# Kernel optimization log

Measured on AMD Instinct MI355X. Metric: run time of the kernel, lower is better.

## Reference

```python
import jax, jax.numpy as jnp
import numpy as np

N = 100000   # nodes
E = 3200000  # edges
F = 128      # num_features
H = 32       # hidden
G = 512      # graphs in batch


def setup_inputs() -> dict:
    key = jax.random.key(0)
    ks = jax.random.split(key, 6)
    x = jax.random.normal(ks[0], (N, F), dtype=jnp.float32)
    edge_index = jax.random.randint(ks[1], (2, E), 0, N, dtype=jnp.int32)
    batch = jnp.sort(jax.random.randint(ks[2], (N,), 0, G, dtype=jnp.int32))
    W1 = jax.random.normal(ks[3], (F, H), dtype=jnp.float32) * 0.05
    b1 = jnp.zeros((H,), dtype=jnp.float32)
    Wg = jax.random.normal(ks[4], (3 * H, 1), dtype=jnp.float32) * 0.05
    bg = jnp.zeros((1,), dtype=jnp.float32)
    return {"x": x, "edge_index": edge_index, "batch": batch,
            "W1": W1, "b1": b1, "Wg": Wg, "bg": bg}


def gcn_conv(x, W, b, edge_index, n):
    # PyG GCNConv: linear transform, add self-loops, symmetric normalization, scatter-add, bias
    h = x @ W  # [N, H]
    loop = jnp.arange(n, dtype=edge_index.dtype)
    src = jnp.concatenate([edge_index[0], loop])
    dst = jnp.concatenate([edge_index[1], loop])
    deg = jax.ops.segment_sum(jnp.ones_like(dst, dtype=h.dtype), dst, num_segments=n)
    dinv = jnp.where(deg > 0, jax.lax.rsqrt(deg), 0.0)
    norm = dinv[src] * dinv[dst]  # [E+N]
    msg = h[src] * norm[:, None]  # gather + scale
    out = jax.ops.segment_sum(msg, dst, num_segments=n)  # scatter-add
    return out + b


def reference(x, edge_index, batch, W1, b1, Wg, bg):
    h = gcn_conv(x, W1, b1, edge_index, N)  # [N, 32]
    h = jax.nn.relu(h)
    s = jax.ops.segment_sum(h, batch, num_segments=G)          # global_add_pool
    cnt = jax.ops.segment_sum(jnp.ones((N, 1), h.dtype), batch, num_segments=G)
    m = s / jnp.maximum(cnt, 1.0)                              # global_mean_pool
    mx = jax.ops.segment_max(h, batch, num_segments=G)         # global_max_pool
    mx = jnp.where(cnt > 0, mx, 0.0)
    g = jnp.concatenate([s, m, mx], axis=1)  # [G, 96]
    return g @ Wg + bg  # [G, 1]
```

## Files before the change

### kernel.cpp

```cpp
#include <hip/hip_runtime.h>
#include <hip/hip_fp16.h>

#define NN 100000
#define NE 3200000
#define NF 128
#define NH 32
#define NG 512
#define NR 196
#define RSZ 512
#define CAP 17408
#define EPB 8192
#define NBE 391
#define PNB 782
#define PRSZ 128

typedef int   v4i __attribute__((ext_vector_type(4)));
typedef float v4f __attribute__((ext_vector_type(4)));

__device__ __forceinline__ __half2 shfl_xor_h2(__half2 v, int m) {
    int iv = *(int*)&v;
    int r = __shfl_xor(iv, m);
    return *(__half2*)&r;
}

__global__ __launch_bounds__(256) void k_cscatter(const int* __restrict__ src,
                                                  const int* __restrict__ dst,
                                                  int* __restrict__ ccur,
                                                  unsigned int* __restrict__ cbucket) {
    __shared__ int h[NR];
    __shared__ int basev[NR];
    for (int i = threadIdx.x; i < NR; i += 256) h[i] = 0;
    __syncthreads();
    int base = blockIdx.x * EPB;
    int lim = NE - base;
    int4 dv[8], sv[8];
    int valid[8];
#pragma unroll
    for (int k = 0; k < 8; ++k) {
        int idx = threadIdx.x + k * 256;
        valid[k] = (idx * 4 < lim);
        if (valid[k]) {
            dv[k] = ((const int4*)(dst + base))[idx];
            sv[k] = ((const int4*)(src + base))[idx];
            atomicAdd(&h[dv[k].x >> 9], 1);
            atomicAdd(&h[dv[k].y >> 9], 1);
            atomicAdd(&h[dv[k].z >> 9], 1);
            atomicAdd(&h[dv[k].w >> 9], 1);
        }
    }
    __syncthreads();
    for (int i = threadIdx.x; i < NR; i += 256) {
        int c = h[i];
        basev[i] = c ? (i * CAP + atomicAdd(&ccur[i], c)) : 0;
    }
    __syncthreads();
    for (int i = threadIdx.x; i < NR; i += 256) h[i] = 0;
    __syncthreads();
#pragma unroll
    for (int k = 0; k < 8; ++k) {
        if (valid[k]) {
            int d, s, r, p;
#define EMIT(DD, SS) d = (DD); s = (SS); r = d >> 9; \
            p = basev[r] + atomicAdd(&h[r], 1); \
            cbucket[p] = (unsigned int)(((d & 511) << 17) | s);
            EMIT(dv[k].x, sv[k].x)
            EMIT(dv[k].y, sv[k].y)
            EMIT(dv[k].z, sv[k].z)
            EMIT(dv[k].w, sv[k].w)
#undef EMIT
        }
    }
}

__global__ __launch_bounds__(256) void k_cscan(const int* __restrict__ ccur,
                                               int* __restrict__ cptr) {
    int t = threadIdx.x;
    int own = (t < NR) ? ccur[t] : 0;
    __shared__ int part[256];
    part[t] = own;
    __syncthreads();
    for (int off = 1; off < 256; off <<= 1) {
        int v = (t >= off) ? part[t - off] : 0;
        __syncthreads();
        part[t] += v;
        __syncthreads();
    }
    if (t < NR) cptr[t] = part[t] - own;
    if (t == 0) cptr[NR] = NE;
}

__global__ __launch_bounds__(512) void k_rangesort(const int* __restrict__ cptr,
                                                   const unsigned int* __restrict__ cbucket,
                                                   int* __restrict__ row_ptr,
                                                   int* __restrict__ bucket,
                                                   float* __restrict__ dinv) {
    __shared__ int h[RSZ];
    __shared__ int lptr[RSZ];
    int r = blockIdx.x;
    int obeg = cptr[r];
    int cnt = cptr[r + 1] - obeg;
    int ibeg = r * CAP;
    int t = threadIdx.x;
    h[t] = 0;
    __syncthreads();
    for (int i = t; i < cnt; i += RSZ)
        atomicAdd(&h[cbucket[ibeg + i] >> 17], 1);
    __syncthreads();
    lptr[t] = h[t];
    __syncthreads();
    for (int off = 1; off < RSZ; off <<= 1) {
        int v = (t >= off) ? lptr[t - off] : 0;
        __syncthreads();
        lptr[t] += v;
        __syncthreads();
    }
    int node0 = r * RSZ;
    int v = node0 + t;
    if (v < NN) {
        int ex = lptr[t] - h[t];
        row_ptr[v] = obeg + ex;
        dinv[v] = rsqrtf((float)(h[t] + 1));
    }
    __syncthreads();
    h[t] = lptr[t] - h[t];
    __syncthreads();
    for (int i = t; i < cnt; i += RSZ) {
        unsigned int w = cbucket[ibeg + i];
        int off_ = atomicAdd(&h[w >> 17], 1);
        bucket[obeg + off_] = (int)(w & 0x1FFFF);
    }
    if (r == 0 && t == 0) row_ptr[NN] = NE;
}

__global__ __launch_bounds__(256) void k_gemm(const float* __restrict__ x,
                                              const float* __restrict__ W1,
                                              const float* __restrict__ dinv,
                                              __half* __restrict__ hs) {
    __shared__ float sW[NF][NH];
    __shared__ float sX[32][NF + 4];
    int t = threadIdx.x;
    const float4* W4 = (const float4*)W1;
    float4* sW4 = (float4*)&sW[0][0];
#pragma unroll
    for (int i = 0; i < 4; ++i) sW4[t + 256 * i] = W4[t + 256 * i];

    long row0 = (long)blockIdx.x * 32;
    const float* xb = x + row0 * NF;
#pragma unroll
    for (int i = 0; i < 4; ++i) {
        int idx4 = t + 256 * i;
        int r = idx4 >> 5;
        int c = (idx4 & 31) * 4;
        v4f v = __builtin_nontemporal_load((const v4f*)(xb + idx4 * 4));
        sX[r][c] = v.x; sX[r][c + 1] = v.y; sX[r][c + 2] = v.z; sX[r][c + 3] = v.w;
    }
    __syncthreads();

    int r = t >> 3;
    int c = (t & 7) * 4;
    float4 acc = {0.f, 0.f, 0.f, 0.f};
#pragma unroll 8
    for (int k = 0; k < NF; ++k) {
        float xv = sX[r][k];
        float4 w = *(const float4*)&sW[k][c];
        acc.x += xv * w.x; acc.y += xv * w.y;
        acc.z += xv * w.z; acc.w += xv * w.w;
    }
    float dv = dinv[row0 + r];
    __half2 h01 = __floats2half2_rn(acc.x * dv, acc.y * dv);
    __half2 h23 = __floats2half2_rn(acc.z * dv, acc.w * dv);
    uint2 packed = { *(unsigned int*)&h01, *(unsigned int*)&h23 };
    *(uint2*)&hs[(row0 + r) * NH + c] = packed;
}

__global__ __launch_bounds__(256) void k_gath(
    const int* __restrict__ row_ptr, const int* __restrict__ bucket,
    const __half* __restrict__ hs, const float* __restrict__ dinv,
    const float* __restrict__ b1, __half* __restrict__ nodeout) {
    int wave = threadIdx.x >> 6;
    int lane = threadIdx.x & 63;
    int fq = lane & 3;
    int es = lane >> 2;
    int v = blockIdx.x * 4 + wave;
    int beg = row_ptr[v], end = row_ptr[v + 1];
    int n = end - beg;
    int bk = 0;
    if (lane < n) bk = bucket[beg + lane];
    float dv = dinv[v];
    uint4 sraw = *(const uint4*)&hs[(size_t)v * NH + fq * 8];

    int u0 = __shfl(bk, es);
    int u1 = __shfl(bk, es + 16);
    int u2 = __shfl(bk, es + 32);
    uint4 r0 = {0, 0, 0, 0}, r1 = {0, 0, 0, 0}, r2 = {0, 0, 0, 0};
    if (es < n)      r0 = *(const uint4*)&hs[(size_t)u0 * NH + fq * 8];
    if (es + 16 < n) r1 = *(const uint4*)&hs[(size_t)u1 * NH + fq * 8];
    if (es + 32 < n) r2 = *(const uint4*)&hs[(size_t)u2 * NH + fq * 8];

    __half2 zero2 = __floats2half2_rn(0.f, 0.f);
    __half2 a0 = zero2, a1 = zero2, a2 = zero2, a3 = zero2;
#define ACC(RR) { \
    a0 = __hadd2(a0, *(__half2*)&RR.x); \
    a1 = __hadd2(a1, *(__half2*)&RR.y); \
    a2 = __hadd2(a2, *(__half2*)&RR.z); \
    a3 = __hadd2(a3, *(__half2*)&RR.w); }
    ACC(r0) ACC(r1) ACC(r2)

    for (int base = 48; base < n; base += 16) {
        int idx = base + es;
        int u = (idx < 64) ? __shfl(bk, idx) : ((idx < n) ? bucket[beg + idx] : 0);
        if (idx < n) {
            uint4 rr = *(const uint4*)&hs[(size_t)u * NH + fq * 8];
            ACC(rr)
        }
    }
#undef ACC

#pragma unroll
    for (int m = 4; m < 64; m <<= 1) {
        a0 = __hadd2(a0, shfl_xor_h2(a0, m));
        a1 = __hadd2(a1, shfl_xor_h2(a1, m));
        a2 = __hadd2(a2, shfl_xor_h2(a2, m));
        a3 = __hadd2(a3, shfl_xor_h2(a3, m));
    }
    if (es == 0) {
        float2 g0 = __half22float2(a0);
        float2 g1 = __half22float2(a1);
        float2 g2 = __half22float2(a2);
        float2 g3 = __half22float2(a3);
        float2 f0 = __half22float2(*(__half2*)&sraw.x);
        float2 f1 = __half22float2(*(__half2*)&sraw.y);
        float2 f2 = __half22float2(*(__half2*)&sraw.z);
        float2 f3 = __half22float2(*(__half2*)&sraw.w);
        float4 bb0 = *(const float4*)&b1[fq * 8];
        float4 bb1 = *(const float4*)&b1[fq * 8 + 4];
        __half2 p0 = __floats2half2_rn(fmaxf((g0.x + f0.x) * dv + bb0.x, 0.f),
                                       fmaxf((g0.y + f0.y) * dv + bb0.y, 0.f));
        __half2 p1 = __floats2half2_rn(fmaxf((g1.x + f1.x) * dv + bb0.z, 0.f),
                                       fmaxf((g1.y + f1.y) * dv + bb0.w, 0.f));
        __half2 p2 = __floats2half2_rn(fmaxf((g2.x + f2.x) * dv + bb1.x, 0.f),
                                       fmaxf((g2.y + f2.y) * dv + bb1.y, 0.f));
        __half2 p3 = __floats2half2_rn(fmaxf((g3.x + f3.x) * dv + bb1.z, 0.f),
                                       fmaxf((g3.y + f3.y) * dv + bb1.w, 0.f));
        v4i pk;
        pk.x = *(int*)&p0; pk.y = *(int*)&p1; pk.z = *(int*)&p2; pk.w = *(int*)&p3;
        __builtin_nontemporal_store(pk, (v4i*)(nodeout + (size_t)v * NH + fq * 8));
    }
}

__global__ __launch_bounds__(256) void k_pool(const __half* __restrict__ nodeout,
                                              const int* __restrict__ batch,
                                              float* __restrict__ s,
                                              unsigned int* __restrict__ mx,
                                              float* __restrict__ cnt) {
    int t = threadIdx.x;
    int f = t & 31;
    int v0 = blockIdx.x * PRSZ + (t >> 5) * 16;
    int curg = -1;
    float rs = 0.f, rm = 0.f, rc = 0.f;
    for (int i = 0; i < 16; ++i) {
        int v = v0 + i;
        if (v >= NN) break;
        int g = batch[v];
        float val = __half2float(nodeout[(size_t)v * NH + f]);
        if (g != curg) {
            if (curg >= 0) {
                atomicAdd(&s[curg * NH + f], rs);
                atomicMax(&mx[curg * NH + f], __float_as_uint(rm));
                if (f == 0) atomicAdd(&cnt[curg], rc);
            }
            curg = g; rs = 0.f; rm = 0.f; rc = 0.f;
        }
        rs += val; rm = fmaxf(rm, val); rc += 1.f;
    }
    if (curg >= 0) {
        atomicAdd(&s[curg * NH + f], rs);
        atomicMax(&mx[curg * NH + f], __float_as_uint(rm));
        if (f == 0) atomicAdd(&cnt[curg], rc);
    }
}

__global__ void k_head(const float* __restrict__ s,
                       const unsigned int* __restrict__ mx,
                       const float* __restrict__ cnt,
                       const float* __restrict__ Wg,
                       const float* __restrict__ bg,
                       float* __restrict__ out) {
    int g = blockIdx.x * blockDim.x + threadIdx.x;
    if (g >= NG) return;
    float inv = 1.0f / fmaxf(cnt[g], 1.0f);
    float accv = bg[0];
#pragma unroll 4
    for (int k = 0; k < NH; ++k) {
        float sv = s[g * NH + k];
        float mv = __uint_as_float(mx[g * NH + k]);
        accv += sv * Wg[k] + sv * inv * Wg[NH + k] + mv * Wg[2 * NH + k];
    }
    out[g] = accv;
}

extern "C" void kernel_launch(void* const* d_in, const int* in_sizes, int n_in,
                              void* d_out, int out_size, void* d_ws, size_t ws_size,
                              hipStream_t stream) {
    const float* x     = (const float*)d_in[0];
    const int*   ei    = (const int*)d_in[1];
    const int*   batch = (const int*)d_in[2];
    const float* W1    = (const float*)d_in[3];
    const float* b1    = (const float*)d_in[4];
    const float* Wg    = (const float*)d_in[5];
    const float* bg    = (const float*)d_in[6];
    float* out = (float*)d_out;

    const int* src = ei;
    const int* dst = ei + NE;

    char* ws = (char*)d_ws;
    int*          ccur    = (int*)(ws + 0);
    int*          cptr    = (int*)(ws + 800);
    int*          row_ptr = (int*)(ws + 1600);
    float*        dinv    = (float*)(ws + 401616);
    int*          bucket  = (int*)(ws + 801616);
    unsigned int* cbucket = (unsigned int*)(ws + 13601664);
    __half*       hs      = (__half*)(ws + 13601664);
    __half*       nodeout = (__half*)(ws + 20001664);
    float*        s       = (float*)(ws + 26401664);
    unsigned int* mx      = (unsigned int*)(ws + 26467200);
    float*        cnt     = (float*)(ws + 26532736);

    hipMemsetAsync(ccur, 0, NR * sizeof(int), stream);

    k_cscatter<<<NBE, 256, 0, stream>>>(src, dst, ccur, cbucket);
    k_cscan<<<1, 256, 0, stream>>>(ccur, cptr);
    k_rangesort<<<NR, RSZ, 0, stream>>>(cptr, cbucket, row_ptr, bucket, dinv);

    hipMemsetAsync(s, 0, (size_t)(NG * NH * 4 + NG * NH * 4 + NG * 4), stream);

    k_gemm<<<NN / 32, 256, 0, stream>>>(x, W1, dinv, hs);
    k_gath<<<NN / 4, 256, 0, stream>>>(row_ptr, bucket, hs, dinv, b1, nodeout);
    k_pool<<<PNB, 256, 0, stream>>>(nodeout, batch, s, mx, cnt);
    k_head<<<(NG + 255) / 256, 256, 0, stream>>>(s, mx, cnt, Wg, bg, out);
}
```

Baseline: 150.1 us.

## Reuse scatter ranks, fold bucket scan into rangesort, zero pool buffers in gather

```diff
diff --git a/kernel.cpp b/kernel.cpp
--- a/kernel.cpp
+++ b/kernel.cpp
@@ -13,6 +13,7 @@
 #define NBE 391
 #define PNB 782
 #define PRSZ 128
+#define ZV4 16512
 
 typedef int   v4i __attribute__((ext_vector_type(4)));
 typedef float v4f __attribute__((ext_vector_type(4)));
@@ -34,6 +35,7 @@
     int base = blockIdx.x * EPB;
     int lim = NE - base;
     int4 dv[8], sv[8];
+    int rank[8][4];
     int valid[8];
 #pragma unroll
     for (int k = 0; k < 8; ++k) {
@@ -42,10 +44,10 @@
         if (valid[k]) {
             dv[k] = ((const int4*)(dst + base))[idx];
             sv[k] = ((const int4*)(src + base))[idx];
-            atomicAdd(&h[dv[k].x >> 9], 1);
-            atomicAdd(&h[dv[k].y >> 9], 1);
-            atomicAdd(&h[dv[k].z >> 9], 1);
-            atomicAdd(&h[dv[k].w >> 9], 1);
+            rank[k][0] = atomicAdd(&h[dv[k].x >> 9], 1);
+            rank[k][1] = atomicAdd(&h[dv[k].y >> 9], 1);
+            rank[k][2] = atomicAdd(&h[dv[k].z >> 9], 1);
+            rank[k][3] = atomicAdd(&h[dv[k].w >> 9], 1);
         }
     }
     __syncthreads();
@@ -54,55 +56,44 @@
         basev[i] = c ? (i * CAP + atomicAdd(&ccur[i], c)) : 0;
     }
     __syncthreads();
-    for (int i = threadIdx.x; i < NR; i += 256) h[i] = 0;
-    __syncthreads();
 #pragma unroll
     for (int k = 0; k < 8; ++k) {
         if (valid[k]) {
             int d, s, r, p;
-#define EMIT(DD, SS) d = (DD); s = (SS); r = d >> 9; \
-            p = basev[r] + atomicAdd(&h[r], 1); \
+#define EMIT(DD, SS, RK) d = (DD); s = (SS); r = d >> 9; \
+            p = basev[r] + (RK); \
             cbucket[p] = (unsigned int)(((d & 511) << 17) | s);
-            EMIT(dv[k].x, sv[k].x)
-            EMIT(dv[k].y, sv[k].y)
-            EMIT(dv[k].z, sv[k].z)
-            EMIT(dv[k].w, sv[k].w)
+            EMIT(dv[k].x, sv[k].x, rank[k][0])
+            EMIT(dv[k].y, sv[k].y, rank[k][1])
+            EMIT(dv[k].z, sv[k].z, rank[k][2])
+            EMIT(dv[k].w, sv[k].w, rank[k][3])
 #undef EMIT
         }
     }
 }
 
-__global__ __launch_bounds__(256) void k_cscan(const int* __restrict__ ccur,
-                                               int* __restrict__ cptr) {
-    int t = threadIdx.x;
-    int own = (t < NR) ? ccur[t] : 0;
-    __shared__ int part[256];
-    part[t] = own;
-    __syncthreads();
-    for (int off = 1; off < 256; off <<= 1) {
-        int v = (t >= off) ? part[t - off] : 0;
-        __syncthreads();
-        part[t] += v;
-        __syncthreads();
-    }
-    if (t < NR) cptr[t] = part[t] - own;
-    if (t == 0) cptr[NR] = NE;
-}
-
-__global__ __launch_bounds__(512) void k_rangesort(const int* __restrict__ cptr,
+__global__ __launch_bounds__(512) void k_rangesort(const int* __restrict__ ccur,
                                                    const unsigned int* __restrict__ cbucket,
                                                    int* __restrict__ row_ptr,
                                                    int* __restrict__ bucket,
                                                    float* __restrict__ dinv) {
+    __shared__ int part[256];
     __shared__ int h[RSZ];
     __shared__ int lptr[RSZ];
     int r = blockIdx.x;
-    int obeg = cptr[r];
-    int cnt = cptr[r + 1] - obeg;
+    int t = threadIdx.x;
+    if (t < 256) part[t] = (t < NR) ? ccur[t] : 0;
+    h[t] = 0;
+    __syncthreads();
+    for (int off = 1; off < 256; off <<= 1) {
+        int v = (t >= off && t < 256) ? part[t - off] : 0;
+        __syncthreads();
+        if (t < 256) part[t] += v;
+        __syncthreads();
+    }
+    int cnt = ccur[r];
+    int obeg = part[r] - cnt;
     int ibeg = r * CAP;
-    int t = threadIdx.x;
-    h[t] = 0;
-    __syncthreads();
     for (int i = t; i < cnt; i += RSZ)
         atomicAdd(&h[cbucket[ibeg + i] >> 17], 1);
     __syncthreads();
@@ -176,7 +167,12 @@
 __global__ __launch_bounds__(256) void k_gath(
     const int* __restrict__ row_ptr, const int* __restrict__ bucket,
     const __half* __restrict__ hs, const float* __restrict__ dinv,
-    const float* __restrict__ b1, __half* __restrict__ nodeout) {
+    const float* __restrict__ b1, __half* __restrict__ nodeout,
+    v4i* __restrict__ szero) {
+    if (blockIdx.x < (ZV4 + 255) / 256) {
+        int idx = blockIdx.x * 256 + threadIdx.x;
+        if (idx < ZV4) { v4i z = {0, 0, 0, 0}; szero[idx] = z; }
+    }
     int wave = threadIdx.x >> 6;
     int lane = threadIdx.x & 63;
     int fq = lane & 3;
@@ -316,7 +312,6 @@
 
     char* ws = (char*)d_ws;
     int*          ccur    = (int*)(ws + 0);
-    int*          cptr    = (int*)(ws + 800);
     int*          row_ptr = (int*)(ws + 1600);
     float*        dinv    = (float*)(ws + 401616);
     int*          bucket  = (int*)(ws + 801616);
@@ -330,13 +325,10 @@
     hipMemsetAsync(ccur, 0, NR * sizeof(int), stream);
 
     k_cscatter<<<NBE, 256, 0, stream>>>(src, dst, ccur, cbucket);
-    k_cscan<<<1, 256, 0, stream>>>(ccur, cptr);
-    k_rangesort<<<NR, RSZ, 0, stream>>>(cptr, cbucket, row_ptr, bucket, dinv);
-
-    hipMemsetAsync(s, 0, (size_t)(NG * NH * 4 + NG * NH * 4 + NG * 4), stream);
-
+    k_rangesort<<<NR, RSZ, 0, stream>>>(ccur, cbucket, row_ptr, bucket, dinv);
     k_gemm<<<NN / 32, 256, 0, stream>>>(x, W1, dinv, hs);
-    k_gath<<<NN / 4, 256, 0, stream>>>(row_ptr, bucket, hs, dinv, b1, nodeout);
+    k_gath<<<NN / 4, 256, 0, stream>>>(row_ptr, bucket, hs, dinv, b1, nodeout,
+                                       (v4i*)s);
     k_pool<<<PNB, 256, 0, stream>>>(nodeout, batch, s, mx, cnt);
     k_head<<<(NG + 255) / 256, 256, 0, stream>>>(s, mx, cnt, Wg, bg, out);
 }
```

Result: no change. 148.1 us (-1.3%).
